# Kernel tuning notes

Measured on AMD Instinct MI355X. Metric: run time of the kernel, lower is better.

Reference implementation:

```python
import jax, jax.numpy as jnp
import numpy as np

B, C, H, W = 2, 128, 64, 64
CR4 = C // 4  # hidden width of linear_weight / bias branches
SOFTMAX_SCALE = 1.0


def _leaky(z):
    return jnp.where(z >= 0, z, 0.2 * z)


def _conv1x1(x, w, b):
    # x: [B,Ci,H,W], w: [Co,Ci], b: [Co]
    return jnp.einsum('oc,bchw->bohw', w, x) + b[None, :, None, None]


def setup_inputs() -> dict:
    key = jax.random.key(0)
    ks = jax.random.split(key, 16)
    def n(k, shape, s=0.05):
        return jax.random.normal(k, shape, jnp.float32) * s
    return {
        'x': jax.random.normal(ks[0], (B, C, H, W), jnp.float32),
        'value_w': n(ks[1], (C, C)), 'value_b': n(ks[2], (C,)),
        'query_w': n(ks[3], (C, C)), 'query_b': n(ks[4], (C,)),
        'lw1_w': n(ks[5], (CR4, C)), 'lw1_b': n(ks[6], (CR4,)),
        'lw2_w': n(ks[7], (1, CR4)), 'lw2_b': n(ks[8], (1,)),
        'bi1_w': n(ks[9], (CR4, C)), 'bi1_b': n(ks[10], (CR4,)),
        'bi2_w': n(ks[11], (1, CR4)), 'bi2_b': n(ks[12], (1,)),
        'lin_w': n(ks[13], (C, C, 3, 3)), 'lin_b': n(ks[14], (C,)),
    }


def reference(x, value_w, value_b, query_w, query_b,
              lw1_w, lw1_b, lw2_w, lw2_b,
              bi1_w, bi1_b, bi2_w, bi2_b,
              lin_w, lin_b):
    # value / query 1x1 projections
    x1 = _conv1x1(x, value_w, value_b)   # [B,C,H,W]
    x2 = _conv1x1(x, query_w, query_b)   # [B,C,H,W]
    # dynamic per-pixel weight / bias maps (two 1x1 convs + LeakyReLU)
    wei = _conv1x1(_leaky(_conv1x1(x2, lw1_w, lw1_b)), lw2_w, lw2_b)  # [B,1,H,W]
    bii = _conv1x1(_leaky(_conv1x1(x2, bi1_w, bi1_b)), bi2_w, bi2_b)  # [B,1,H,W]

    Bn, Cn, Hn, Wn = x.shape
    L = Hn * Wn  # one 1x1 patch per spatial location (ksize=1, stride=1)
    # query patches [B,L,C]; normalize each patch to (at least 1e-4) unit norm
    wq = x2.transpose(0, 2, 3, 1).reshape(Bn, L, Cn)
    wnorm = wq / jnp.maximum(jnp.linalg.norm(wq, axis=2, keepdims=True), 1e-4)
    # attention scores: per-sample conv2d(xi, wi_normed) == batched matmul
    yi = jnp.einsum('bchw,blc->blhw', x2, wnorm)  # [B,L,H,W]
    # sparse gating
    sparse = jax.nn.relu(yi - yi.mean(axis=1, keepdims=True) * wei + bii)
    sr = (sparse != 0.0).astype(yi.dtype)
    yi = yi * sparse
    yi = jax.nn.softmax(yi * SOFTMAX_SCALE, axis=1)
    yi = jnp.maximum(yi * sr, 1e-8)
    # reconstruct with value patches (conv_transpose2d with 1x1 kernels)
    raw = x1.transpose(0, 2, 3, 1).reshape(Bn, L, Cn)
    out = jnp.einsum('blhw,blc->bchw', yi, raw)  # / (ksize*ksize) == /1
    # final 3x3 conv + LeakyReLU + residual
    y = jax.lax.conv_general_dilated(out, lin_w, (1, 1), 'SAME',
                                     dimension_numbers=('NCHW', 'OIHW', 'NCHW'))
    y = _leaky(y + lin_b[None, :, None, None])
    return y + x
```

## Files before the change

### kernel.cpp

```cpp
#include <hip/hip_runtime.h>
#include <hip/hip_bf16.h>
#include <math.h>

#define BB 2
#define C 128
#define L 4096
#define CR4 32
#define RS 4

typedef unsigned short ushort_t;
typedef __attribute__((ext_vector_type(8))) short s16x8;
typedef __attribute__((ext_vector_type(4))) float f32x4;

__device__ inline float leaky(float z) { return (z >= 0.f) ? z : 0.2f * z; }

__device__ inline unsigned short f2bf(float f) {
    unsigned int u = __builtin_bit_cast(unsigned int, f);
    unsigned int r = (u + 0x7fffu + ((u >> 16) & 1u)) >> 16;
    return (unsigned short)r;
}
__device__ inline float bf2f(unsigned short b) {
    unsigned int u = ((unsigned int)b) << 16;
    return __builtin_bit_cast(float, u);
}
__device__ inline unsigned int cvtpk(float lo, float hi) {
    unsigned int r;
    asm("v_cvt_pk_bf16_f32 %0, %1, %2" : "=v"(r) : "v"(lo), "v"(hi));
    return r;
}

__global__ __launch_bounds__(256) void k_wcomp(
    const float* __restrict__ vw, const float* __restrict__ vb,
    const float* __restrict__ qw, const float* __restrict__ qb,
    const float* __restrict__ lw1w, const float* __restrict__ lw1b,
    const float* __restrict__ bi1w, const float* __restrict__ bi1b,
    ushort_t* __restrict__ WQV, float* __restrict__ biasv)
{
    const int mt = blockIdx.x;
    const int t = threadIdx.x;
    const int kk = t >> 6, lane = t & 63;
    const int row = mt * 16 + (lane & 15);
    const int k0 = kk * 32 + (lane >> 4) * 8;
    s16x8 v;
    if (row < 128) {
        #pragma unroll
        for (int j = 0; j < 8; ++j) v[j] = (short)f2bf(vw[row * 128 + k0 + j]);
    } else if (row < 256) {
        #pragma unroll
        for (int j = 0; j < 8; ++j) v[j] = (short)f2bf(qw[(row - 128) * 128 + k0 + j]);
    } else {
        const float* w1 = (row < 288) ? lw1w + (row - 256) * 128
                                      : bi1w + (row - 288) * 128;
        float acc[8] = {0.f, 0.f, 0.f, 0.f, 0.f, 0.f, 0.f, 0.f};
        #pragma unroll 2
        for (int k = 0; k < 128; ++k) {
            float wv_ = w1[k];
            const float* qr = qw + k * 128 + k0;
            #pragma unroll
            for (int j = 0; j < 8; ++j) acc[j] = fmaf(wv_, qr[j], acc[j]);
        }
        #pragma unroll
        for (int j = 0; j < 8; ++j) v[j] = (short)f2bf(acc[j]);
    }
    *(s16x8*)(WQV + ((size_t)(mt * 4 + kk) * 64 + lane) * 8) = v;

    if (t < 16) {
        int rr = mt * 16 + t;
        float bv;
        if (rr < 128) bv = vb[rr];
        else if (rr < 256) bv = qb[rr - 128];
        else {
            const float* w1 = (rr < 288) ? lw1w + (rr - 256) * 128
                                         : bi1w + (rr - 288) * 128;
            float a = (rr < 288) ? lw1b[rr - 256] : bi1b[rr - 288];
            for (int k = 0; k < 128; ++k) a = fmaf(w1[k], qb[k], a);
            bv = a;
        }
        biasv[rr] = bv;
    }
}

__global__ __launch_bounds__(256, 1) void k_proj2(
    const float* __restrict__ x, const ushort_t* __restrict__ WQV,
    const float* __restrict__ biasv,
    const float* __restrict__ lw2w, const float* __restrict__ lw2b,
    const float* __restrict__ bi2w, const float* __restrict__ bi2b,
    ushort_t* __restrict__ x2a, ushort_t* __restrict__ x1g,
    float* __restrict__ weiA, float* __restrict__ biiA, float* __restrict__ scA,
    float* __restrict__ cpart)
{
    __shared__ __align__(16) char smem[16384 + 1536];
    char* xT = smem;
    float* biasLDS = (float*)(smem + 16384);
    float* w2LDS = biasLDS + 320;

    const int t = threadIdx.x;
    const int blk = blockIdx.x;
    const int b = blk >> 6;
    const int p0 = (blk & 63) * 64;
    const int wv = t >> 6, lane = t & 63, n = lane & 15, g = lane >> 4;

    biasLDS[t] = biasv[t];
    if (t < 64) {
        biasLDS[256 + t] = biasv[256 + t];
        w2LDS[t] = (t < 32) ? lw2w[t] : bi2w[t - 32];
    }

    const int pl = t & 63, cg = t >> 6;
    const float* xb = x + (size_t)b * C * L + p0 + pl;
    #pragma unroll
    for (int i = 0; i < 16; ++i) {
        int c = cg * 32 + i * 2;
        float v0 = xb[(size_t)c * L];
        float v1 = xb[(size_t)(c + 1) * L];
        int slot = c >> 3;
        int offs = (c * 2) & 15;
        int byte = pl * 256 + (((slot ^ (pl & 15)) << 4) | offs);
        *(unsigned int*)(xT + byte) = cvtpk(v0, v1);
    }
    __syncthreads();

    f32x4 acc[20];
    #pragma unroll
    for (int mt = 0; mt < 20; ++mt) acc[mt] = (f32x4){0.f, 0.f, 0.f, 0.f};

    const int brow = wv * 16 + n;
    #pragma unroll
    for (int kk = 0; kk < 4; ++kk) {
        const s16x8 bfr = *(const s16x8*)(xT + brow * 256 + (((4 * kk + g) ^ n) << 4));
        #pragma unroll
        for (int mt = 0; mt < 20; ++mt) {
            const s16x8 afr = *(const s16x8*)(WQV + ((size_t)(mt * 4 + kk) * 64 + lane) * 8);
            acc[mt] = __builtin_amdgcn_mfma_f32_16x16x32_bf16(afr, bfr, acc[mt], 0, 0, 0);
        }
    }

    #pragma unroll
    for (int mt = 0; mt < 20; ++mt) {
        const f32x4 bv = *(const f32x4*)(biasLDS + mt * 16 + g * 4);
        acc[mt][0] += bv[0]; acc[mt][1] += bv[1];
        acc[mt][2] += bv[2]; acc[mt][3] += bv[3];
    }

    const int p = p0 + wv * 16 + n;
    const size_t bL = (size_t)b * L;

    float pn = 0.f;
    #pragma unroll
    for (int mt = 8; mt < 16; ++mt)
        #pragma unroll
        for (int r = 0; r < 4; ++r) pn = fmaf(acc[mt][r], acc[mt][r], pn);
    pn += __shfl_xor(pn, 16, 64);
    pn += __shfl_xor(pn, 32, 64);
    float scv = fmaxf(sqrtf(pn), 1e-4f);
    float dinv = 1.f / scv;

    float pw = 0.f, pbb = 0.f;
    #pragma unroll
    for (int mt = 16; mt < 18; ++mt)
        #pragma unroll
        for (int r = 0; r < 4; ++r)
            pw = fmaf(w2LDS[(mt - 16) * 16 + g * 4 + r], leaky(acc[mt][r]), pw);
    #pragma unroll
    for (int mt = 18; mt < 20; ++mt)
        #pragma unroll
        for (int r = 0; r < 4; ++r)
            pbb = fmaf(w2LDS[32 + (mt - 18) * 16 + g * 4 + r], leaky(acc[mt][r]), pbb);
    pw += __shfl_xor(pw, 16, 64);  pw += __shfl_xor(pw, 32, 64);
    pbb += __shfl_xor(pbb, 16, 64); pbb += __shfl_xor(pbb, 32, 64);

    if (g == 0) {
        weiA[bL + p] = pw + lw2b[0];
        biiA[bL + p] = pbb + bi2b[0];
        scA[bL + p]  = scv;
    }

    #pragma unroll
    for (int mt = 8; mt < 16; ++mt) {
        uint2 uu;
        uu.x = cvtpk(acc[mt][0] * dinv, acc[mt][1] * dinv);
        uu.y = cvtpk(acc[mt][2] * dinv, acc[mt][3] * dinv);
        *(uint2*)(x2a + (bL + p) * C + (mt - 8) * 16 + g * 4) = uu;
    }
    #pragma unroll
    for (int mt = 0; mt < 8; ++mt)
        #pragma unroll
        for (int r = 0; r < 4; ++r)
            x1g[((size_t)b * C + mt * 16 + g * 4 + r) * L + p] = f2bf(acc[mt][r]);

    float sv[32];
    #pragma unroll
    for (int mt = 8; mt < 16; ++mt)
        #pragma unroll
        for (int r = 0; r < 4; ++r)
            sv[(mt - 8) * 4 + r] = acc[mt][r] * dinv;
    #pragma unroll
    for (int mask = 1; mask <= 8; mask <<= 1)
        #pragma unroll
        for (int i = 0; i < 32; ++i)
            sv[i] += __shfl_xor(sv[i], mask, 64);

    __syncthreads();
    float* sumsh = (float*)xT;
    if (n == 0) {
        #pragma unroll
        for (int i = 0; i < 32; ++i) {
            int ch = (i >> 2) * 16 + g * 4 + (i & 3);
            sumsh[wv * 128 + ch] = sv[i];
        }
    }
    __syncthreads();
    if (t < 128)
        cpart[(size_t)blk * 128 + t] =
            (sumsh[t] + sumsh[128 + t]) + (sumsh[256 + t] + sumsh[384 + t]);
}

__global__ __launch_bounds__(128) void k_cb(
    const float* __restrict__ cpart, float* __restrict__ cbv)
{
    const int b = blockIdx.x, t = threadIdx.x;
    float s = 0.f;
    #pragma unroll 4
    for (int j = 0; j < 64; ++j) s += cpart[(size_t)(b * 64 + j) * 128 + t];
    cbv[b * 128 + t] = s * (1.f / (float)L);
}

__global__ __launch_bounds__(256, 2) void k_attn(
    const ushort_t* __restrict__ x2a, const ushort_t* __restrict__ x1g,
    const float* __restrict__ scA, const float* __restrict__ weiA,
    const float* __restrict__ biiA, const float* __restrict__ cbv,
    ushort_t* __restrict__ Opb, float* __restrict__ Mp, float* __restrict__ Zp)
{
    __shared__ __align__(16) char smem[53248];

    const int t = threadIdx.x;
    const int w = t >> 6, lane = t & 63, n = lane & 15, g = lane >> 4;
    char* Pw = smem + 49152 + w * 1024;

    const int blk = blockIdx.x;
    const int xcd = blk & 7;
    const int b = xcd >> 2;
    const int ti = (xcd & 3) * 64 + (blk >> 3);
    const int q = ti & 3;
    const int colt = ti >> 2;
    const int p = colt * 64 + w * 16 + n;
    const size_t bL = (size_t)b * L;

    const s16x8* qrow = (const s16x8*)(x2a + (bL + p) * C);
    const float scp = scA[bL + p];
    s16x8 bq[4];
    float dot = 0.f;
    #pragma unroll
    for (int kk = 0; kk < 4; ++kk) {
        s16x8 raw = qrow[kk * 4 + g];
        const float* cbp = cbv + b * 128 + kk * 32 + g * 8;
        s16x8 u;
        #pragma unroll
        for (int j = 0; j < 8; ++j) {
            float rv = bf2f((unsigned short)raw[j]) * scp;
            u[j] = (short)f2bf(rv);
            dot = fmaf(cbp[j], rv, dot);
        }
        bq[kk] = u;
    }
    dot += __shfl_xor(dot, 16, 64);
    dot += __shfl_xor(dot, 32, 64);
    const float tq = fmaf(weiA[bL + p], dot, -biiA[bL + p]);

    f32x4 Oacc[8];
    #pragma unroll
    for (int ct = 0; ct < 8; ++ct) Oacc[ct] = (f32x4){0.f, 0.f, 0.f, 0.f};
    float Mrun = 0.f, Zrun = 0.f;

    const int l0base = q * (L / RS);
    const char* x2src = (const char*)(x2a + (bL + l0base) * C);
    const char* x1src = (const char*)(x1g + (size_t)b * C * L);

    #define STAGE_X2(buf, tile_)                                                         \
        {   const char* sb = x2src + (size_t)(tile_) * 32 * 256;                          \
            _Pragma("unroll")                                                             \
            for (int rr = 0; rr < 2; ++rr) {                                              \
                int slot = rr * 256 + t;                                                  \
                int lrow = slot >> 4, uu = slot & 15;                                     \
                const char* gp = sb + lrow * 256 + (((uu ^ (lrow & 7))) << 4);            \
                char* lp = (buf) + ((rr * 256 + w * 64) << 4);                            \
                __builtin_amdgcn_global_load_lds(                                         \
                    (const __attribute__((address_space(1))) unsigned int*)gp,            \
                    (__attribute__((address_space(3))) unsigned int*)lp, 16, 0, 0);       \
            } }
    #define STAGE_X1(buf, l0_)                                                            \
        {   _Pragma("unroll")                                                             \
            for (int rr = 0; rr < 2; ++rr) {                                              \
                int slot = rr * 256 + t;                                                  \
                int cr = slot >> 2, uu = slot & 3;                                        \
                const char* gp = x1src + ((size_t)cr * L + (l0_)) * 2 + ((uu ^ (cr & 3)) << 4); \
                char* lp = (buf) + ((rr * 256 + w * 64) << 4);                            \
                __builtin_amdgcn_global_load_lds(                                         \
                    (const __attribute__((address_space(1))) unsigned int*)gp,            \
                    (__attribute__((address_space(3))) unsigned int*)lp, 16, 0, 0);       \
            } }

    const int NT = (L / RS) / 32;

    STAGE_X2(smem, 0);
    STAGE_X1(smem + 24576, l0base);
    STAGE_X2(smem + 8192, 1);
    STAGE_X1(smem + 24576 + 8192, l0base + 32);
    asm volatile("s_waitcnt vmcnt(4)" ::: "memory");
    __builtin_amdgcn_s_barrier();
    asm volatile("" ::: "memory");

    const int swzA = n & 7;
    const int swzX = n & 3;

    int cur = 0;
    #pragma unroll 1
    for (int tile = 0; tile < NT; ++tile) {
        int nx2 = cur + 2; if (nx2 >= 3) nx2 -= 3;
        if (tile + 2 < NT) {
            STAGE_X2(smem + nx2 * 8192, tile + 2);
            STAGE_X1(smem + 24576 + nx2 * 8192, l0base + (tile + 2) * 32);
        }
        char* Ab = smem + cur * 8192;
        char* Xb = smem + 24576 + cur * 8192;

        f32x4 s4[2];
        s4[0] = (f32x4){0.f, 0.f, 0.f, 0.f};
        s4[1] = (f32x4){0.f, 0.f, 0.f, 0.f};
        __builtin_amdgcn_s_setprio(1);
        #pragma unroll
        for (int kk = 0; kk < 4; ++kk) {
            #pragma unroll
            for (int lt = 0; lt < 2; ++lt) {
                const s16x8 a_ = *(const s16x8*)(Ab + (16 * lt + n) * 256 +
                                                 (((4 * kk + g) ^ swzA) << 4));
                s4[lt] = __builtin_amdgcn_mfma_f32_16x16x32_bf16(a_, bq[kk], s4[lt], 0, 0, 0);
            }
        }
        __builtin_amdgcn_s_setprio(0);

        float vv[8], sps[8];
        #pragma unroll
        for (int lt = 0; lt < 2; ++lt) {
            #pragma unroll
            for (int r = 0; r < 4; ++r) {
                float s = s4[lt][r];
                float sp = s - tq;
                sps[lt * 4 + r] = sp;
                vv[lt * 4 + r] = s * fmaxf(sp, 0.f);
            }
        }
        float tm0 = fmaxf(fmaxf(vv[0], vv[1]), fmaxf(vv[2], vv[3]));
        float tm1 = fmaxf(fmaxf(vv[4], vv[5]), fmaxf(vv[6], vv[7]));
        float tmax = fmaxf(tm0, tm1);
        tmax = fmaxf(tmax, __shfl_xor(tmax, 16, 64));
        tmax = fmaxf(tmax, __shfl_xor(tmax, 32, 64));

        if (!__all(tmax <= Mrun + 8.f)) {
            float Mn = fmaxf(Mrun, tmax);
            float so = __expf(Mrun - Mn);
            Mrun = Mn;
            Zrun *= so;
            #pragma unroll
            for (int ct = 0; ct < 8; ++ct) {
                Oacc[ct][0] *= so; Oacc[ct][1] *= so;
                Oacc[ct][2] *= so; Oacc[ct][3] *= so;
            }
        }

        #pragma unroll
        for (int lt = 0; lt < 2; ++lt) {
            float e0 = __expf(vv[lt * 4 + 0] - Mrun);
            float e1 = __expf(vv[lt * 4 + 1] - Mrun);
            float e2 = __expf(vv[lt * 4 + 2] - Mrun);
            float e3 = __expf(vv[lt * 4 + 3] - Mrun);
            Zrun += (e0 + e1) + (e2 + e3);
            float p0 = sps[lt * 4 + 0] > 0.f ? e0 : 0.f;
            float p1 = sps[lt * 4 + 1] > 0.f ? e1 : 0.f;
            float p2 = sps[lt * 4 + 2] > 0.f ? e2 : 0.f;
            float p3 = sps[lt * 4 + 3] > 0.f ? e3 : 0.f;
            int gt = 2 * lt + (g >> 1);
            int byte = n * 64 + ((gt ^ swzX) << 4) + ((g & 1) << 3);
            uint2 uu;
            uu.x = cvtpk(p0, p1);
            uu.y = cvtpk(p2, p3);
            *(uint2*)(Pw + byte) = uu;
        }

        const s16x8 pb = *(const s16x8*)(Pw + n * 64 + ((g ^ swzX) << 4));
        __builtin_amdgcn_s_setprio(1);
        #pragma unroll
        for (int ct = 0; ct < 8; ++ct) {
            const s16x8 xf_ = *(const s16x8*)(Xb + (16 * ct + n) * 64 +
                                              ((g ^ swzX) << 4));
            Oacc[ct] = __builtin_amdgcn_mfma_f32_16x16x32_bf16(xf_, pb, Oacc[ct], 0, 0, 0);
        }
        __builtin_amdgcn_s_setprio(0);

        if (tile + 2 < NT) {
            asm volatile("s_waitcnt vmcnt(4)" ::: "memory");
        } else {
            asm volatile("s_waitcnt vmcnt(0)" ::: "memory");
        }
        __builtin_amdgcn_s_barrier();
        asm volatile("" ::: "memory");

        cur += 1; if (cur == 3) cur = 0;
    }
    #undef STAGE_X2
    #undef STAGE_X1

    float z = Zrun;
    z += __shfl_xor(z, 16, 64);
    z += __shfl_xor(z, 32, 64);

    const size_t sset = (size_t)(q * BB + b);
    ushort_t* ob = Opb + (sset * L + p) * C;
    #pragma unroll
    for (int ct = 0; ct < 8; ++ct) {
        uint2 uu;
        uu.x = cvtpk(Oacc[ct][0], Oacc[ct][1]);
        uu.y = cvtpk(Oacc[ct][2], Oacc[ct][3]);
        *(uint2*)(ob + 16 * ct + 4 * g) = uu;
    }
    if (g == 0) {
        Mp[sset * L + p] = Mrun;
        Zp[sset * L + p] = z;
    }
}

__global__ __launch_bounds__(256) void k_merge(
    const ushort_t* __restrict__ Opb, const float* __restrict__ Mp,
    const float* __restrict__ Zp, ushort_t* __restrict__ attnb)
{
    const int idx = blockIdx.x * 256 + threadIdx.x;
    const int c4 = idx & 31;
    const int p = (idx >> 5) & 4095;
    const int b = idx >> 17;
    size_t is[RS];
    float M = -1e30f;
    float Mq[RS], Zq[RS];
    #pragma unroll
    for (int q = 0; q < RS; ++q) {
        is[q] = (size_t)(q * BB + b) * L + p;
        Mq[q] = Mp[is[q]];
        Zq[q] = Zp[is[q]];
        M = fmaxf(M, Mq[q]);
    }
    float Zt = 0.f;
    float aq[RS];
    #pragma unroll
    for (int q = 0; q < RS; ++q) {
        aq[q] = __expf(Mq[q] - M);
        Zt = fmaf(Zq[q], aq[q], Zt);
    }
    float zi = 1.f / Zt;
    float r0 = 0.f, r1 = 0.f, r2 = 0.f, r3 = 0.f;
    #pragma unroll
    for (int q = 0; q < RS; ++q) {
        float s = aq[q] * zi;
        const ushort4 o = *(const ushort4*)(Opb + is[q] * C + c4 * 4);
        r0 = fmaf(bf2f(o.x), s, r0);
        r1 = fmaf(bf2f(o.y), s, r1);
        r2 = fmaf(bf2f(o.z), s, r2);
        r3 = fmaf(bf2f(o.w), s, r3);
    }
    uint2 uu;
    uu.x = cvtpk(r0, r1);
    uu.y = cvtpk(r2, r3);
    *(uint2*)(attnb + ((size_t)b * L + p) * C + c4 * 4) = uu;
}

__global__ __launch_bounds__(256) void k_wrep(
    const float* __restrict__ lw, ushort_t* __restrict__ W3)
{
    const int tid = blockIdx.x * 256 + threadIdx.x;
    const int s = tid >> 9;
    const int r = tid & 511;
    const int mt = r >> 6, lane = r & 63;
    const int co = mt * 16 + (lane & 15), g = lane >> 4;
    const int kk = s >> 2, kc = s & 3;
    const int ci0 = kc * 32 + g * 8;
    s16x8 v;
    #pragma unroll
    for (int j = 0; j < 8; ++j)
        v[j] = (short)f2bf(lw[((size_t)co * 128 + ci0 + j) * 9 + kk]);
    *(s16x8*)(W3 + (size_t)tid * 8) = v;
}

__global__ __launch_bounds__(256, 1) void k_conv(
    const ushort_t* __restrict__ attnb, const float* __restrict__ x,
    const ushort_t* __restrict__ W3, const float* __restrict__ lb,
    float* __restrict__ out)
{
    __shared__ __align__(16) char smem[65536];
    char* attnT = smem;
    char* Wb0 = smem + 49152;
    char* Wb1 = smem + 57344;

    const int t = threadIdx.x;
    const int wv = t >> 6, lane = t & 63, n = lane & 15, g = lane >> 4;
    const int h = blockIdx.x;
    const int half = blockIdx.y;
    const int b = blockIdx.z;

    const char* asrc = (const char*)attnb + ((size_t)b * L + (size_t)(h - 1) * 64) * C * 2;
    #pragma unroll
    for (int rr = 0; rr < 3; ++rr) {
        if ((unsigned)(h - 1 + rr) < 64u) {
            #pragma unroll
            for (int qq = 0; qq < 4; ++qq) {
                int slot = rr * 1024 + qq * 256 + t;
                int lrow = slot >> 4, uu = slot & 15;
                const char* gp = asrc + lrow * 256 + ((uu ^ (lrow & 7)) << 4);
                char* lp = attnT + ((rr * 1024 + qq * 256 + wv * 64) << 4);
                __builtin_amdgcn_global_load_lds(
                    (const __attribute__((address_space(1))) unsigned int*)gp,
                    (__attribute__((address_space(3))) unsigned int*)lp, 16, 0, 0);
            }
        }
    }
    #define STAGE_W(buf, s_)                                                              \
        {   _Pragma("unroll")                                                             \
            for (int qq = 0; qq < 2; ++qq) {                                              \
                const char* gp = (const char*)W3 + ((size_t)(s_) * 512 + qq * 256 + t) * 16; \
                char* lp = (buf) + ((qq * 256 + wv * 64) << 4);                           \
                __builtin_amdgcn_global_load_lds(                                         \
                    (const __attribute__((address_space(1))) unsigned int*)gp,            \
                    (__attribute__((address_space(3))) unsigned int*)lp, 16, 0, 0);       \
            } }

    STAGE_W(Wb0, 0);
    __syncthreads();

    f32x4 acc[2][2];
    #pragma unroll
    for (int mi = 0; mi < 2; ++mi)
        #pragma unroll
        for (int nt = 0; nt < 2; ++nt) acc[mi][nt] = (f32x4){0.f, 0.f, 0.f, 0.f};

    const s16x8 zer = {0, 0, 0, 0, 0, 0, 0, 0};

    #pragma unroll 1
    for (int s = 0; s < 36; ++s) {
        char* Wc = (s & 1) ? Wb1 : Wb0;
        if (s + 1 < 36) {
            char* Wn = (s & 1) ? Wb0 : Wb1;
            STAGE_W(Wn, s + 1);
        }
        const int kk = s >> 2, kc = s & 3;
        const int kh = kk / 3, kw = kk - kh * 3;
        const int dh = kh - 1, dw = kw - 1;
        const bool hval = ((unsigned)(h + dh) < 64u);

        s16x8 af0 = *(const s16x8*)(Wc + (((2 * wv) * 64 + lane) << 4));
        s16x8 af1 = *(const s16x8*)(Wc + (((2 * wv + 1) * 64 + lane) << 4));

        #pragma unroll
        for (int nt = 0; nt < 2; ++nt) {
            int pl = half * 32 + nt * 16 + n;
            int wd = pl + dw;
            bool val = hval && ((unsigned)wd < 64u);
            int wc = wd < 0 ? 0 : (wd > 63 ? 63 : wd);
            int lrow = (dh + 1) * 64 + wc;
            s16x8 bf_ = *(const s16x8*)(attnT + lrow * 256 +
                                        (((kc * 4 + g) ^ (lrow & 7)) << 4));
            if (!val) bf_ = zer;
            acc[0][nt] = __builtin_amdgcn_mfma_f32_16x16x32_bf16(af0, bf_, acc[0][nt], 0, 0, 0);
            acc[1][nt] = __builtin_amdgcn_mfma_f32_16x16x32_bf16(af1, bf_, acc[1][nt], 0, 0, 0);
        }
        __syncthreads();
    }
    #undef STAGE_W

    const float* xb = x + (size_t)b * C * L + h * 64;
    float* ob = out + (size_t)b * C * L + h * 64;
    #pragma unroll
    for (int mi = 0; mi < 2; ++mi) {
        #pragma unroll
        for (int r = 0; r < 4; ++r) {
            int co = (2 * wv + mi) * 16 + g * 4 + r;
            float bias = lb[co];
            #pragma unroll
            for (int nt = 0; nt < 2; ++nt) {
                int p_ = half * 32 + nt * 16 + n;
                float v = leaky(acc[mi][nt][r] + bias);
                ob[(size_t)co * L + p_] = v + xb[(size_t)co * L + p_];
            }
        }
    }
}

extern "C" void kernel_launch(void* const* d_in, const int* in_sizes, int n_in,
                              void* d_out, int out_size, void* d_ws, size_t ws_size,
                              hipStream_t stream) {
    const float* x     = (const float*)d_in[0];
    const float* vw    = (const float*)d_in[1];
    const float* vb    = (const float*)d_in[2];
    const float* qw    = (const float*)d_in[3];
    const float* qb    = (const float*)d_in[4];
    const float* lw1w  = (const float*)d_in[5];
    const float* lw1b  = (const float*)d_in[6];
    const float* lw2w  = (const float*)d_in[7];
    const float* lw2b  = (const float*)d_in[8];
    const float* bi1w  = (const float*)d_in[9];
    const float* bi1b  = (const float*)d_in[10];
    const float* bi2w  = (const float*)d_in[11];
    const float* bi2b  = (const float*)d_in[12];
    const float* lw    = (const float*)d_in[13];
    const float* lb    = (const float*)d_in[14];
    float* out = (float*)d_out;

    char* ws = (char*)d_ws;
    ushort_t* x2a  = (ushort_t*)ws;
    ushort_t* x1g  = (ushort_t*)(ws + 2097152);
    ushort_t* Opb  = (ushort_t*)(ws + 4194304);
    ushort_t* WQV  = (ushort_t*)(ws + 4194304);
    float* biasv = (float*)(ws + 4194304 + 81920);
    float* weiA  = (float*)(ws + 12582912);
    float* biiA  = weiA + BB * L;
    float* scA   = biiA + BB * L;
    float* Mp    = scA + BB * L;
    float* Zp    = Mp + RS * BB * L;
    float* cpart = Zp + RS * BB * L;
    float* cbv   = cpart + 128 * 128;
    ushort_t* W3 = x1g;
    ushort_t* attnb = x2a;

    hipLaunchKernelGGL(k_wcomp, dim3(20), dim3(256), 0, stream,
                       vw, vb, qw, qb, lw1w, lw1b, bi1w, bi1b, WQV, biasv);

    hipLaunchKernelGGL(k_proj2, dim3(BB * (L / 64)), dim3(256), 0, stream,
                       x, WQV, biasv, lw2w, lw2b, bi2w, bi2b,
                       x2a, x1g, weiA, biiA, scA, cpart);

    hipLaunchKernelGGL(k_cb, dim3(BB), dim3(128), 0, stream, cpart, cbv);

    hipLaunchKernelGGL(k_attn, dim3(BB * 64 * RS), dim3(256), 0, stream,
                       x2a, x1g, scA, weiA, biiA, cbv, Opb, Mp, Zp);

    hipLaunchKernelGGL(k_wrep, dim3(72), dim3(256), 0, stream, lw, W3);

    hipLaunchKernelGGL(k_merge, dim3(BB * L * C / 4 / 256), dim3(256), 0, stream,
                       Opb, Mp, Zp, attnb);

    hipLaunchKernelGGL(k_conv, dim3(64, 2, BB), dim3(256), 0, stream,
                       attnb, x, W3, lb, out);
}
```

Before: 110.8 us.

## Split projection kernel across two block halves and retile attention to 64-wide double buffer

The projection kernel now launches a second grid dimension: one half computes the value projection plus the weight/bias branches, the other computes the normalized query, its norm and the channel partial sums. This doubles the block count and lowers per-block register pressure, at the cost of loading and transposing x twice. The attention kernel moves from a 3-stage ring of 32-key tiles with manual vmcnt waits to a 2-stage double buffer of 64-key tiles with plain __syncthreads, using more LDS per block. It also drops the XCD-aware block-index remapping in favour of a linear mapping.

New measurement: 105.4 us. 4.8% less time.

```diff
diff --git a/kernel.cpp b/kernel.cpp
--- a/kernel.cpp
+++ b/kernel.cpp
@@ -96,6 +96,7 @@
 
     const int t = threadIdx.x;
     const int blk = blockIdx.x;
+    const int part = blockIdx.y;
     const int b = blk >> 6;
     const int p0 = (blk & 63) * 64;
     const int wv = t >> 6, lane = t & 63, n = lane & 15, g = lane >> 4;
@@ -120,99 +121,113 @@
     }
     __syncthreads();
 
-    f32x4 acc[20];
-    #pragma unroll
-    for (int mt = 0; mt < 20; ++mt) acc[mt] = (f32x4){0.f, 0.f, 0.f, 0.f};
-
     const int brow = wv * 16 + n;
-    #pragma unroll
-    for (int kk = 0; kk < 4; ++kk) {
-        const s16x8 bfr = *(const s16x8*)(xT + brow * 256 + (((4 * kk + g) ^ n) << 4));
-        #pragma unroll
-        for (int mt = 0; mt < 20; ++mt) {
-            const s16x8 afr = *(const s16x8*)(WQV + ((size_t)(mt * 4 + kk) * 64 + lane) * 8);
-            acc[mt] = __builtin_amdgcn_mfma_f32_16x16x32_bf16(afr, bfr, acc[mt], 0, 0, 0);
-        }
-    }
-
-    #pragma unroll
-    for (int mt = 0; mt < 20; ++mt) {
-        const f32x4 bv = *(const f32x4*)(biasLDS + mt * 16 + g * 4);
-        acc[mt][0] += bv[0]; acc[mt][1] += bv[1];
-        acc[mt][2] += bv[2]; acc[mt][3] += bv[3];
-    }
-
     const int p = p0 + wv * 16 + n;
     const size_t bL = (size_t)b * L;
 
-    float pn = 0.f;
-    #pragma unroll
-    for (int mt = 8; mt < 16; ++mt)
-        #pragma unroll
-        for (int r = 0; r < 4; ++r) pn = fmaf(acc[mt][r], acc[mt][r], pn);
-    pn += __shfl_xor(pn, 16, 64);
-    pn += __shfl_xor(pn, 32, 64);
-    float scv = fmaxf(sqrtf(pn), 1e-4f);
-    float dinv = 1.f / scv;
-
-    float pw = 0.f, pbb = 0.f;
-    #pragma unroll
-    for (int mt = 16; mt < 18; ++mt)
-        #pragma unroll
-        for (int r = 0; r < 4; ++r)
-            pw = fmaf(w2LDS[(mt - 16) * 16 + g * 4 + r], leaky(acc[mt][r]), pw);
-    #pragma unroll
-    for (int mt = 18; mt < 20; ++mt)
-        #pragma unroll
-        for (int r = 0; r < 4; ++r)
-            pbb = fmaf(w2LDS[32 + (mt - 18) * 16 + g * 4 + r], leaky(acc[mt][r]), pbb);
-    pw += __shfl_xor(pw, 16, 64);  pw += __shfl_xor(pw, 32, 64);
-    pbb += __shfl_xor(pbb, 16, 64); pbb += __shfl_xor(pbb, 32, 64);
-
-    if (g == 0) {
-        weiA[bL + p] = pw + lw2b[0];
-        biiA[bL + p] = pbb + bi2b[0];
-        scA[bL + p]  = scv;
-    }
-
-    #pragma unroll
-    for (int mt = 8; mt < 16; ++mt) {
-        uint2 uu;
-        uu.x = cvtpk(acc[mt][0] * dinv, acc[mt][1] * dinv);
-        uu.y = cvtpk(acc[mt][2] * dinv, acc[mt][3] * dinv);
-        *(uint2*)(x2a + (bL + p) * C + (mt - 8) * 16 + g * 4) = uu;
-    }
-    #pragma unroll
-    for (int mt = 0; mt < 8; ++mt)
-        #pragma unroll
-        for (int r = 0; r < 4; ++r)
-            x1g[((size_t)b * C + mt * 16 + g * 4 + r) * L + p] = f2bf(acc[mt][r]);
-
-    float sv[32];
-    #pragma unroll
-    for (int mt = 8; mt < 16; ++mt)
-        #pragma unroll
-        for (int r = 0; r < 4; ++r)
-            sv[(mt - 8) * 4 + r] = acc[mt][r] * dinv;
-    #pragma unroll
-    for (int mask = 1; mask <= 8; mask <<= 1)
-        #pragma unroll
-        for (int i = 0; i < 32; ++i)
-            sv[i] += __shfl_xor(sv[i], mask, 64);
-
-    __syncthreads();
-    float* sumsh = (float*)xT;
-    if (n == 0) {
-        #pragma unroll
-        for (int i = 0; i < 32; ++i) {
-            int ch = (i >> 2) * 16 + g * 4 + (i & 3);
-            sumsh[wv * 128 + ch] = sv[i];
-        }
-    }
-    __syncthreads();
-    if (t < 128)
-        cpart[(size_t)blk * 128 + t] =
-            (sumsh[t] + sumsh[128 + t]) + (sumsh[256 + t] + sumsh[384 + t]);
+    if (part == 0) {
+        const int mtm[12] = {0, 1, 2, 3, 4, 5, 6, 7, 16, 17, 18, 19};
+        f32x4 acc[12];
+        #pragma unroll
+        for (int i = 0; i < 12; ++i) acc[i] = (f32x4){0.f, 0.f, 0.f, 0.f};
+        #pragma unroll
+        for (int kk = 0; kk < 4; ++kk) {
+            const s16x8 bfr = *(const s16x8*)(xT + brow * 256 + (((4 * kk + g) ^ n) << 4));
+            #pragma unroll
+            for (int i = 0; i < 12; ++i) {
+                const s16x8 afr = *(const s16x8*)(WQV + ((size_t)(mtm[i] * 4 + kk) * 64 + lane) * 8);
+                acc[i] = __builtin_amdgcn_mfma_f32_16x16x32_bf16(afr, bfr, acc[i], 0, 0, 0);
+            }
+        }
+        #pragma unroll
+        for (int i = 0; i < 12; ++i) {
+            const f32x4 bv = *(const f32x4*)(biasLDS + mtm[i] * 16 + g * 4);
+            acc[i][0] += bv[0]; acc[i][1] += bv[1];
+            acc[i][2] += bv[2]; acc[i][3] += bv[3];
+        }
+        #pragma unroll
+        for (int i = 0; i < 8; ++i)
+            #pragma unroll
+            for (int r = 0; r < 4; ++r)
+                x1g[((size_t)b * C + i * 16 + g * 4 + r) * L + p] = f2bf(acc[i][r]);
+        float pw = 0.f, pbb = 0.f;
+        #pragma unroll
+        for (int i = 8; i < 10; ++i)
+            #pragma unroll
+            for (int r = 0; r < 4; ++r)
+                pw = fmaf(w2LDS[(i - 8) * 16 + g * 4 + r], leaky(acc[i][r]), pw);
+        #pragma unroll
+        for (int i = 10; i < 12; ++i)
+            #pragma unroll
+            for (int r = 0; r < 4; ++r)
+                pbb = fmaf(w2LDS[32 + (i - 10) * 16 + g * 4 + r], leaky(acc[i][r]), pbb);
+        pw += __shfl_xor(pw, 16, 64);  pw += __shfl_xor(pw, 32, 64);
+        pbb += __shfl_xor(pbb, 16, 64); pbb += __shfl_xor(pbb, 32, 64);
+        if (g == 0) {
+            weiA[bL + p] = pw + lw2b[0];
+            biiA[bL + p] = pbb + bi2b[0];
+        }
+    } else {
+        f32x4 acc[8];
+        #pragma unroll
+        for (int i = 0; i < 8; ++i) acc[i] = (f32x4){0.f, 0.f, 0.f, 0.f};
+        #pragma unroll
+        for (int kk = 0; kk < 4; ++kk) {
+            const s16x8 bfr = *(const s16x8*)(xT + brow * 256 + (((4 * kk + g) ^ n) << 4));
+            #pragma unroll
+            for (int i = 0; i < 8; ++i) {
+                const s16x8 afr = *(const s16x8*)(WQV + ((size_t)((8 + i) * 4 + kk) * 64 + lane) * 8);
+                acc[i] = __builtin_amdgcn_mfma_f32_16x16x32_bf16(afr, bfr, acc[i], 0, 0, 0);
+            }
+        }
+        #pragma unroll
+        for (int i = 0; i < 8; ++i) {
+            const f32x4 bv = *(const f32x4*)(biasLDS + (8 + i) * 16 + g * 4);
+            acc[i][0] += bv[0]; acc[i][1] += bv[1];
+            acc[i][2] += bv[2]; acc[i][3] += bv[3];
+        }
+        float pn = 0.f;
+        #pragma unroll
+        for (int i = 0; i < 8; ++i)
+            #pragma unroll
+            for (int r = 0; r < 4; ++r) pn = fmaf(acc[i][r], acc[i][r], pn);
+        pn += __shfl_xor(pn, 16, 64);
+        pn += __shfl_xor(pn, 32, 64);
+        float scv = fmaxf(sqrtf(pn), 1e-4f);
+        float dinv = 1.f / scv;
+        if (g == 0) scA[bL + p] = scv;
+        #pragma unroll
+        for (int i = 0; i < 8; ++i) {
+            uint2 uu;
+            uu.x = cvtpk(acc[i][0] * dinv, acc[i][1] * dinv);
+            uu.y = cvtpk(acc[i][2] * dinv, acc[i][3] * dinv);
+            *(uint2*)(x2a + (bL + p) * C + i * 16 + g * 4) = uu;
+        }
+        float sv[32];
+        #pragma unroll
+        for (int i = 0; i < 8; ++i)
+            #pragma unroll
+            for (int r = 0; r < 4; ++r)
+                sv[i * 4 + r] = acc[i][r] * dinv;
+        #pragma unroll
+        for (int mask = 1; mask <= 8; mask <<= 1)
+            #pragma unroll
+            for (int i = 0; i < 32; ++i)
+                sv[i] += __shfl_xor(sv[i], mask, 64);
+        __syncthreads();
+        float* sumsh = (float*)xT;
+        if (n == 0) {
+            #pragma unroll
+            for (int i = 0; i < 32; ++i) {
+                int ch = (i >> 2) * 16 + g * 4 + (i & 3);
+                sumsh[wv * 128 + ch] = sv[i];
+            }
+        }
+        __syncthreads();
+        if (t < 128)
+            cpart[(size_t)blk * 128 + t] =
+                (sumsh[t] + sumsh[128 + t]) + (sumsh[256 + t] + sumsh[384 + t]);
+    }
 }
 
 __global__ __launch_bounds__(128) void k_cb(
@@ -231,18 +246,16 @@
     const float* __restrict__ biiA, const float* __restrict__ cbv,
     ushort_t* __restrict__ Opb, float* __restrict__ Mp, float* __restrict__ Zp)
 {
-    __shared__ __align__(16) char smem[53248];
+    __shared__ __align__(16) char smem[73728];
 
     const int t = threadIdx.x;
     const int w = t >> 6, lane = t & 63, n = lane & 15, g = lane >> 4;
-    char* Pw = smem + 49152 + w * 1024;
+    char* Pw = smem + 65536 + w * 2048;
 
     const int blk = blockIdx.x;
-    const int xcd = blk & 7;
-    const int b = xcd >> 2;
-    const int ti = (xcd & 3) * 64 + (blk >> 3);
-    const int q = ti & 3;
-    const int colt = ti >> 2;
+    const int q = blk & (RS - 1);
+    const int colt = (blk >> 2) & 63;
+    const int b = blk >> 8;
     const int p = colt * 64 + w * 16 + n;
     const size_t bL = (size_t)b * L;
 
@@ -277,9 +290,9 @@
     const char* x1src = (const char*)(x1g + (size_t)b * C * L);
 
     #define STAGE_X2(buf, tile_)                                                         \
-        {   const char* sb = x2src + (size_t)(tile_) * 32 * 256;                          \
+        {   const char* sb = x2src + (size_t)(tile_) * 64 * 256;                          \
             _Pragma("unroll")                                                             \
-            for (int rr = 0; rr < 2; ++rr) {                                              \
+            for (int rr = 0; rr < 4; ++rr) {                                              \
                 int slot = rr * 256 + t;                                                  \
                 int lrow = slot >> 4, uu = slot & 15;                                     \
                 const char* gp = sb + lrow * 256 + (((uu ^ (lrow & 7))) << 4);            \
@@ -290,58 +303,55 @@
             } }
     #define STAGE_X1(buf, l0_)                                                            \
         {   _Pragma("unroll")                                                             \
-            for (int rr = 0; rr < 2; ++rr) {                                              \
+            for (int rr = 0; rr < 4; ++rr) {                                              \
                 int slot = rr * 256 + t;                                                  \
-                int cr = slot >> 2, uu = slot & 3;                                        \
-                const char* gp = x1src + ((size_t)cr * L + (l0_)) * 2 + ((uu ^ (cr & 3)) << 4); \
+                int cr = slot >> 3, uu = slot & 7;                                        \
+                const char* gp = x1src + ((size_t)cr * L + (l0_) + ((uu ^ (cr & 7)) << 3)) * 2; \
                 char* lp = (buf) + ((rr * 256 + w * 64) << 4);                            \
                 __builtin_amdgcn_global_load_lds(                                         \
                     (const __attribute__((address_space(1))) unsigned int*)gp,            \
                     (__attribute__((address_space(3))) unsigned int*)lp, 16, 0, 0);       \
             } }
 
-    const int NT = (L / RS) / 32;
-
-    STAGE_X2(smem, 0);
-    STAGE_X1(smem + 24576, l0base);
-    STAGE_X2(smem + 8192, 1);
-    STAGE_X1(smem + 24576 + 8192, l0base + 32);
-    asm volatile("s_waitcnt vmcnt(4)" ::: "memory");
-    __builtin_amdgcn_s_barrier();
-    asm volatile("" ::: "memory");
-
-    const int swzA = n & 7;
-    const int swzX = n & 3;
-
-    int cur = 0;
+    char* Abuf0 = smem;          char* Abuf1 = smem + 16384;
+    char* Xbuf0 = smem + 32768;  char* Xbuf1 = smem + 49152;
+
+    STAGE_X2(Abuf0, 0);
+    STAGE_X1(Xbuf0, l0base);
+    __syncthreads();
+
+    const int swz = n & 7;
+    const int NT = L / RS / 64;
+
     #pragma unroll 1
     for (int tile = 0; tile < NT; ++tile) {
-        int nx2 = cur + 2; if (nx2 >= 3) nx2 -= 3;
-        if (tile + 2 < NT) {
-            STAGE_X2(smem + nx2 * 8192, tile + 2);
-            STAGE_X1(smem + 24576 + nx2 * 8192, l0base + (tile + 2) * 32);
-        }
-        char* Ab = smem + cur * 8192;
-        char* Xb = smem + 24576 + cur * 8192;
-
-        f32x4 s4[2];
-        s4[0] = (f32x4){0.f, 0.f, 0.f, 0.f};
-        s4[1] = (f32x4){0.f, 0.f, 0.f, 0.f};
+        char* Ab = (tile & 1) ? Abuf1 : Abuf0;
+        char* Xb = (tile & 1) ? Xbuf1 : Xbuf0;
+        if (tile + 1 < NT) {
+            char* An = (tile & 1) ? Abuf0 : Abuf1;
+            char* Xn = (tile & 1) ? Xbuf0 : Xbuf1;
+            STAGE_X2(An, tile + 1);
+            STAGE_X1(Xn, l0base + (tile + 1) * 64);
+        }
+
+        f32x4 s4[4];
+        #pragma unroll
+        for (int lt = 0; lt < 4; ++lt) s4[lt] = (f32x4){0.f, 0.f, 0.f, 0.f};
         __builtin_amdgcn_s_setprio(1);
         #pragma unroll
         for (int kk = 0; kk < 4; ++kk) {
             #pragma unroll
-            for (int lt = 0; lt < 2; ++lt) {
-                const s16x8 a_ = *(const s16x8*)(Ab + (16 * lt + n) * 256 +
-                                                 (((4 * kk + g) ^ swzA) << 4));
-                s4[lt] = __builtin_amdgcn_mfma_f32_16x16x32_bf16(a_, bq[kk], s4[lt], 0, 0, 0);
+            for (int lt = 0; lt < 4; ++lt) {
+                const s16x8 a = *(const s16x8*)(Ab + (16 * lt + n) * 256 +
+                                                (((4 * kk + g) ^ swz) << 4));
+                s4[lt] = __builtin_amdgcn_mfma_f32_16x16x32_bf16(a, bq[kk], s4[lt], 0, 0, 0);
             }
         }
         __builtin_amdgcn_s_setprio(0);
 
-        float vv[8], sps[8];
-        #pragma unroll
-        for (int lt = 0; lt < 2; ++lt) {
+        float vv[16], sps[16];
+        #pragma unroll
+        for (int lt = 0; lt < 4; ++lt) {
             #pragma unroll
             for (int r = 0; r < 4; ++r) {
                 float s = s4[lt][r];
@@ -350,9 +360,12 @@
                 vv[lt * 4 + r] = s * fmaxf(sp, 0.f);
             }
         }
-        float tm0 = fmaxf(fmaxf(vv[0], vv[1]), fmaxf(vv[2], vv[3]));
-        float tm1 = fmaxf(fmaxf(vv[4], vv[5]), fmaxf(vv[6], vv[7]));
-        float tmax = fmaxf(tm0, tm1);
+        float tm[8];
+        #pragma unroll
+        for (int i = 0; i < 8; ++i) tm[i] = fmaxf(vv[2 * i], vv[2 * i + 1]);
+        #pragma unroll
+        for (int i = 0; i < 4; ++i) tm[i] = fmaxf(tm[2 * i], tm[2 * i + 1]);
+        float tmax = fmaxf(fmaxf(tm[0], tm[1]), fmaxf(tm[2], tm[3]));
         tmax = fmaxf(tmax, __shfl_xor(tmax, 16, 64));
         tmax = fmaxf(tmax, __shfl_xor(tmax, 32, 64));
 
@@ -369,7 +382,7 @@
         }
 
         #pragma unroll
-        for (int lt = 0; lt < 2; ++lt) {
+        for (int lt = 0; lt < 4; ++lt) {
             float e0 = __expf(vv[lt * 4 + 0] - Mrun);
             float e1 = __expf(vv[lt * 4 + 1] - Mrun);
             float e2 = __expf(vv[lt * 4 + 2] - Mrun);
@@ -379,33 +392,27 @@
             float p1 = sps[lt * 4 + 1] > 0.f ? e1 : 0.f;
             float p2 = sps[lt * 4 + 2] > 0.f ? e2 : 0.f;
             float p3 = sps[lt * 4 + 3] > 0.f ? e3 : 0.f;
-            int gt = 2 * lt + (g >> 1);
-            int byte = n * 64 + ((gt ^ swzX) << 4) + ((g & 1) << 3);
+            int ulog = 2 * lt + (g >> 1);
+            int byte = n * 128 + ((ulog ^ swz) << 4) + ((g & 1) << 3);
             uint2 uu;
             uu.x = cvtpk(p0, p1);
             uu.y = cvtpk(p2, p3);
             *(uint2*)(Pw + byte) = uu;
         }
 
-        const s16x8 pb = *(const s16x8*)(Pw + n * 64 + ((g ^ swzX) << 4));
         __builtin_amdgcn_s_setprio(1);
         #pragma unroll
-        for (int ct = 0; ct < 8; ++ct) {
-            const s16x8 xf_ = *(const s16x8*)(Xb + (16 * ct + n) * 64 +
-                                              ((g ^ swzX) << 4));
-            Oacc[ct] = __builtin_amdgcn_mfma_f32_16x16x32_bf16(xf_, pb, Oacc[ct], 0, 0, 0);
+        for (int kk2 = 0; kk2 < 2; ++kk2) {
+            const s16x8 pb = *(const s16x8*)(Pw + n * 128 + (((4 * kk2 + g) ^ swz) << 4));
+            #pragma unroll
+            for (int ct = 0; ct < 8; ++ct) {
+                const s16x8 a = *(const s16x8*)(Xb + (16 * ct + n) * 128 +
+                                                (((4 * kk2 + g) ^ swz) << 4));
+                Oacc[ct] = __builtin_amdgcn_mfma_f32_16x16x32_bf16(a, pb, Oacc[ct], 0, 0, 0);
+            }
         }
         __builtin_amdgcn_s_setprio(0);
-
-        if (tile + 2 < NT) {
-            asm volatile("s_waitcnt vmcnt(4)" ::: "memory");
-        } else {
-            asm volatile("s_waitcnt vmcnt(0)" ::: "memory");
-        }
-        __builtin_amdgcn_s_barrier();
-        asm volatile("" ::: "memory");
-
-        cur += 1; if (cur == 3) cur = 0;
+        __syncthreads();
     }
     #undef STAGE_X2
     #undef STAGE_X1
@@ -630,7 +637,7 @@
     hipLaunchKernelGGL(k_wcomp, dim3(20), dim3(256), 0, stream,
                        vw, vb, qw, qb, lw1w, lw1b, bi1w, bi1b, WQV, biasv);
 
-    hipLaunchKernelGGL(k_proj2, dim3(BB * (L / 64)), dim3(256), 0, stream,
+    hipLaunchKernelGGL(k_proj2, dim3(128, 2), dim3(256), 0, stream,
                        x, WQV, biasv, lw2w, lw2b, bi2w, bi2b,
                        x2a, x1g, weiA, biiA, scA, cpart);
 
```
